# Kernel optimization log

Hardware: AMD Instinct MI355X
Metric: run time of the kernel (lower is better)

## Reference

```python
import jax, jax.numpy as jnp
import numpy as np

N_NODES = 50000
N_EDGES = 800000
HIDDEN = 128
BN_EPS = 1e-5


def setup_inputs() -> dict:
    key = jax.random.key(0)
    k_h, k_e, k_wl, k_wr = jax.random.split(key, 4)
    h = jax.random.normal(k_h, (N_NODES, HIDDEN), dtype=jnp.float32)
    edge_index = jax.random.randint(k_e, (2, N_EDGES), 0, N_NODES, dtype=jnp.int32)
    W_l = jax.random.normal(k_wl, (HIDDEN, HIDDEN), dtype=jnp.float32) / np.sqrt(HIDDEN)
    b_l = jnp.zeros((HIDDEN,), dtype=jnp.float32)
    W_r = jax.random.normal(k_wr, (HIDDEN, HIDDEN), dtype=jnp.float32) / np.sqrt(HIDDEN)
    gamma = jnp.ones((HIDDEN,), dtype=jnp.float32)
    beta = jnp.zeros((HIDDEN,), dtype=jnp.float32)
    return {"h": h, "edge_index": edge_index, "W_l": W_l, "b_l": b_l,
            "W_r": W_r, "gamma": gamma, "beta": beta}


def reference(h, edge_index, W_l, b_l, W_r, gamma, beta):
    # SAGEConv(aggr='mean'): out_i = W_l @ mean_{j->i} h_j + b_l + W_r @ h_i
    src = edge_index[0]  # message sources
    dst = edge_index[1]  # message targets
    n = h.shape[0]
    msg_sum = jax.ops.segment_sum(h[src], dst, num_segments=n)          # [N, D]
    deg = jax.ops.segment_sum(jnp.ones_like(dst, dtype=h.dtype), dst, num_segments=n)
    agg = msg_sum / jnp.maximum(deg, 1.0)[:, None]                      # mean aggregation
    out = agg @ W_l.T + b_l + h @ W_r.T                                 # [N, D]
    # BatchNorm1d (training mode: batch statistics, biased variance)
    mean = jnp.mean(out, axis=0)
    var = jnp.var(out, axis=0)
    out = gamma * (out - mean) * jax.lax.rsqrt(var + BN_EPS) + beta
    out = jax.nn.relu(out)
    # dropout p=0.0 -> identity; residual add
    return out + h
```

## Files before the change

kernel.cpp:

```cpp
#include <hip/hip_runtime.h>

#define N_NODES 50000
#define N_EDGES 800000
#define HIDDEN  128
#define BN_EPS  1e-5f
#define SLOT    64

__global__ __launch_bounds__(256) void bin_kernel(
    const int* __restrict__ edge_index,
    int* __restrict__ cnt,
    int* __restrict__ slots,
    float* __restrict__ bn_acc)
{
    if (blockIdx.x == 0) bn_acc[threadIdx.x] = 0.0f;

    const int* src = edge_index;
    const int* dst = edge_index + N_EDGES;
    const int e = blockIdx.x * blockDim.x + threadIdx.x;
    if (e < N_EDGES) {
        const int d = dst[e];
        const int s = src[e];
        const int pos = atomicAdd(&cnt[d], 1);
        if (pos < SLOT) slots[(size_t)d * SLOT + pos] = s;
    }
}

__global__ __launch_bounds__(256) void gather_kernel(
    const float* __restrict__ h,
    const int* __restrict__ cnt,
    const int* __restrict__ slots,
    float* __restrict__ agg)
{
    const int lane = threadIdx.x & 63;
    const int wave = (blockIdx.x * blockDim.x + threadIdx.x) >> 6;
    if (wave >= N_NODES) return;
    const int n = wave;

    int c = cnt[n];
    c = (c > SLOT) ? SLOT : c;
    const int* sl = slots + (size_t)n * SLOT;
    const int fo = lane * 2;

    float2 acc = make_float2(0.0f, 0.0f);
    int j = 0;
    for (; j + 8 <= c; j += 8) {
        int s0 = sl[j], s1 = sl[j+1], s2 = sl[j+2], s3 = sl[j+3];
        int s4 = sl[j+4], s5 = sl[j+5], s6 = sl[j+6], s7 = sl[j+7];
        float2 v0 = *reinterpret_cast<const float2*>(h + (size_t)s0 * HIDDEN + fo);
        float2 v1 = *reinterpret_cast<const float2*>(h + (size_t)s1 * HIDDEN + fo);
        float2 v2 = *reinterpret_cast<const float2*>(h + (size_t)s2 * HIDDEN + fo);
        float2 v3 = *reinterpret_cast<const float2*>(h + (size_t)s3 * HIDDEN + fo);
        float2 v4 = *reinterpret_cast<const float2*>(h + (size_t)s4 * HIDDEN + fo);
        float2 v5 = *reinterpret_cast<const float2*>(h + (size_t)s5 * HIDDEN + fo);
        float2 v6 = *reinterpret_cast<const float2*>(h + (size_t)s6 * HIDDEN + fo);
        float2 v7 = *reinterpret_cast<const float2*>(h + (size_t)s7 * HIDDEN + fo);
        acc.x += (v0.x + v1.x) + (v2.x + v3.x) + ((v4.x + v5.x) + (v6.x + v7.x));
        acc.y += (v0.y + v1.y) + (v2.y + v3.y) + ((v4.y + v5.y) + (v6.y + v7.y));
    }
    for (; j < c; j++) {
        const int s0 = sl[j];
        const float2 v0 = *reinterpret_cast<const float2*>(h + (size_t)s0 * HIDDEN + fo);
        acc.x += v0.x;
        acc.y += v0.y;
    }
    const float inv = 1.0f / (float)((c > 0) ? c : 1);
    acc.x *= inv;
    acc.y *= inv;
    *reinterpret_cast<float2*>(agg + (size_t)n * HIDDEN + fo) = acc;
}

#define BR 64
#define BC 128
#define KC 16

__global__ __launch_bounds__(256) void gemm_kernel(
    const float* __restrict__ agg,
    const float* __restrict__ h,
    const float* __restrict__ W_l,
    const float* __restrict__ b_l,
    const float* __restrict__ W_r,
    float* __restrict__ out,
    float* __restrict__ bn_acc)
{
    __shared__ float Xs[KC][BR];
    __shared__ float Ws[KC][BC];
    __shared__ float red[16][BC];

    const int tid  = threadIdx.x;
    const int row0 = blockIdx.x * BR;
    const int ty = tid >> 4;
    const int tx = tid & 15;

    float acc[4][8];
#pragma unroll
    for (int i = 0; i < 4; i++)
#pragma unroll
        for (int j = 0; j < 8; j++) acc[i][j] = 0.0f;

    const int srow = tid >> 2;
    const int sq   = (tid & 3) * 4;
    const int wcol = tid >> 1;
    const int wq   = (tid & 1) * 8;

    for (int kc = 0; kc < 2 * HIDDEN; kc += KC) {
        const float* X = (kc < HIDDEN) ? agg : h;
        const float* W = (kc < HIDDEN) ? W_l : W_r;
        const int kb = (kc & (HIDDEN - 1));

        {
            const int r = row0 + srow;
            float4 v = make_float4(0.f, 0.f, 0.f, 0.f);
            if (r < N_NODES)
                v = *reinterpret_cast<const float4*>(X + (size_t)r * HIDDEN + kb + sq);
            Xs[sq + 0][srow] = v.x; Xs[sq + 1][srow] = v.y;
            Xs[sq + 2][srow] = v.z; Xs[sq + 3][srow] = v.w;
        }
        {
            const float4* p = reinterpret_cast<const float4*>(W + (size_t)wcol * HIDDEN + kb + wq);
            float4 a = p[0], b = p[1];
            Ws[wq + 0][wcol] = a.x; Ws[wq + 1][wcol] = a.y;
            Ws[wq + 2][wcol] = a.z; Ws[wq + 3][wcol] = a.w;
            Ws[wq + 4][wcol] = b.x; Ws[wq + 5][wcol] = b.y;
            Ws[wq + 6][wcol] = b.z; Ws[wq + 7][wcol] = b.w;
        }
        __syncthreads();

#pragma unroll
        for (int kk = 0; kk < KC; kk++) {
            float4 av = *reinterpret_cast<const float4*>(&Xs[kk][ty * 4]);
            float4 b0 = *reinterpret_cast<const float4*>(&Ws[kk][tx * 4]);
            float4 b1 = *reinterpret_cast<const float4*>(&Ws[kk][64 + tx * 4]);
            float a[4] = {av.x, av.y, av.z, av.w};
            float b[8] = {b0.x, b0.y, b0.z, b0.w, b1.x, b1.y, b1.z, b1.w};
#pragma unroll
            for (int i = 0; i < 4; i++)
#pragma unroll
                for (int j = 0; j < 8; j++)
                    acc[i][j] += a[i] * b[j];
        }
        __syncthreads();
    }

    float4 bb0 = *reinterpret_cast<const float4*>(&b_l[tx * 4]);
    float4 bb1 = *reinterpret_cast<const float4*>(&b_l[64 + tx * 4]);
    float s[8], s2[8];
#pragma unroll
    for (int j = 0; j < 8; j++) { s[j] = 0.0f; s2[j] = 0.0f; }

#pragma unroll
    for (int i = 0; i < 4; i++) {
        const int r = row0 + ty * 4 + i;
        if (r < N_NODES) {
            float o[8];
            o[0] = acc[i][0] + bb0.x; o[1] = acc[i][1] + bb0.y;
            o[2] = acc[i][2] + bb0.z; o[3] = acc[i][3] + bb0.w;
            o[4] = acc[i][4] + bb1.x; o[5] = acc[i][5] + bb1.y;
            o[6] = acc[i][6] + bb1.z; o[7] = acc[i][7] + bb1.w;
            float* op = out + (size_t)r * HIDDEN;
            *reinterpret_cast<float4*>(op + tx * 4)      = make_float4(o[0], o[1], o[2], o[3]);
            *reinterpret_cast<float4*>(op + 64 + tx * 4) = make_float4(o[4], o[5], o[6], o[7]);
#pragma unroll
            for (int j = 0; j < 8; j++) { s[j] += o[j]; s2[j] += o[j] * o[j]; }
        }
    }

#pragma unroll
    for (int j = 0; j < 4; j++) {
        red[ty][tx * 4 + j]      = s[j];
        red[ty][64 + tx * 4 + j] = s[4 + j];
    }
    __syncthreads();
    if (tid < BC) {
        float t = 0.0f;
#pragma unroll
        for (int y = 0; y < 16; y++) t += red[y][tid];
        atomicAdd(&bn_acc[tid], t);
    }
    __syncthreads();
#pragma unroll
    for (int j = 0; j < 4; j++) {
        red[ty][tx * 4 + j]      = s2[j];
        red[ty][64 + tx * 4 + j] = s2[4 + j];
    }
    __syncthreads();
    if (tid < BC) {
        float t = 0.0f;
#pragma unroll
        for (int y = 0; y < 16; y++) t += red[y][tid];
        atomicAdd(&bn_acc[BC + tid], t);
    }
}

__global__ __launch_bounds__(256) void bn_apply_kernel(
    const float* __restrict__ h,
    const float* __restrict__ gamma,
    const float* __restrict__ beta,
    const float* __restrict__ bn_acc,
    float* __restrict__ out)
{
    const float inv_n = 1.0f / (float)N_NODES;
    const size_t total = (size_t)N_NODES * HIDDEN;
    size_t idx = ((size_t)blockIdx.x * blockDim.x + threadIdx.x) * 4;
    const size_t stride = (size_t)gridDim.x * blockDim.x * 4;

    for (; idx < total; idx += stride) {
        const int col = (int)(idx & (HIDDEN - 1));
        float4 x  = *reinterpret_cast<float4*>(out + idx);
        float4 sm = *reinterpret_cast<const float4*>(bn_acc + col);
        float4 sq = *reinterpret_cast<const float4*>(bn_acc + HIDDEN + col);
        float4 g  = *reinterpret_cast<const float4*>(gamma + col);
        float4 bt = *reinterpret_cast<const float4*>(beta + col);
        float4 hr = *reinterpret_cast<const float4*>(h + idx);

        float4 res;
        {
            float m = sm.x * inv_n; float var = sq.x * inv_n - m * m;
            float rs = rsqrtf(var + BN_EPS);
            float v = g.x * (x.x - m) * rs + bt.x;
            res.x = fmaxf(v, 0.0f) + hr.x;
        }
        {
            float m = sm.y * inv_n; float var = sq.y * inv_n - m * m;
            float rs = rsqrtf(var + BN_EPS);
            float v = g.y * (x.y - m) * rs + bt.y;
            res.y = fmaxf(v, 0.0f) + hr.y;
        }
        {
            float m = sm.z * inv_n; float var = sq.z * inv_n - m * m;
            float rs = rsqrtf(var + BN_EPS);
            float v = g.z * (x.z - m) * rs + bt.z;
            res.z = fmaxf(v, 0.0f) + hr.z;
        }
        {
            float m = sm.w * inv_n; float var = sq.w * inv_n - m * m;
            float rs = rsqrtf(var + BN_EPS);
            float v = g.w * (x.w - m) * rs + bt.w;
            res.w = fmaxf(v, 0.0f) + hr.w;
        }
        *reinterpret_cast<float4*>(out + idx) = res;
    }
}

extern "C" void kernel_launch(void* const* d_in, const int* in_sizes, int n_in,
                              void* d_out, int out_size, void* d_ws, size_t ws_size,
                              hipStream_t stream)
{
    const float* h          = (const float*)d_in[0];
    const int*   edge_index = (const int*)d_in[1];
    const float* W_l        = (const float*)d_in[2];
    const float* b_l        = (const float*)d_in[3];
    const float* W_r        = (const float*)d_in[4];
    const float* gamma      = (const float*)d_in[5];
    const float* beta       = (const float*)d_in[6];
    float* out = (float*)d_out;

    char* ws = (char*)d_ws;
    int*   cnt    = (int*)ws;
    int*   slots  = cnt + N_NODES;
    float* agg    = (float*)(slots + (size_t)N_NODES * SLOT);
    float* bn_acc = agg + (size_t)N_NODES * HIDDEN;

    hipMemsetAsync(cnt, 0, (size_t)N_NODES * sizeof(int), stream);

    bin_kernel<<<(N_EDGES + 255) / 256, 256, 0, stream>>>(edge_index, cnt, slots, bn_acc);

    gather_kernel<<<(N_NODES + 3) / 4, 256, 0, stream>>>(h, cnt, slots, agg);

    const int gemm_blocks = (N_NODES + BR - 1) / BR;
    gemm_kernel<<<gemm_blocks, 256, 0, stream>>>(agg, h, W_l, b_l, W_r, out, bn_acc);

    bn_apply_kernel<<<2048, 256, 0, stream>>>(h, gamma, beta, bn_acc, out);
}
```

Baseline: 258.5 us.

## Use split-bf16 MFMA GEMM with pre-split weights and half-wave gather

Replaces the FP32 SIMT GEMM with bf16 MFMA 16x16x32 instructions, using a hi/lo split (three MFMAs per tile) to keep near-FP32 accuracy. The weights are pre-split into bf16 hi/lo arrays inside the binning kernel and staged in XOR-swizzled shared memory. Activations are converted to hi/lo on the fly. The gather kernel now assigns one node per half-wave with float4 loads, and BN partial sums go through shared-memory atomics. The tradeoff is three times as many matrix ops plus conversion work and non-coalesced scalar output stores, in exchange for matrix-core throughput.

```diff
diff --git a/kernel.cpp b/kernel.cpp
--- a/kernel.cpp
+++ b/kernel.cpp
@@ -6,20 +6,49 @@
 #define BN_EPS  1e-5f
 #define SLOT    64
 
+typedef __attribute__((ext_vector_type(8))) short short8;
+typedef __attribute__((ext_vector_type(4))) float f32x4;
+
+__device__ inline unsigned short f2bf(float x) {
+    unsigned u = __float_as_uint(x);
+    return (unsigned short)((u + 0x7FFFu + ((u >> 16) & 1u)) >> 16);
+}
+__device__ inline void cvt8(const float* x, short8& hi, short8& lo) {
+#pragma unroll
+    for (int i = 0; i < 8; i++) {
+        unsigned u = __float_as_uint(x[i]);
+        unsigned r = (u + 0x7FFFu + ((u >> 16) & 1u)) & 0xFFFF0000u;
+        hi[i] = (short)(r >> 16);
+        float res = x[i] - __uint_as_float(r);
+        lo[i] = (short)f2bf(res);
+    }
+}
+
 __global__ __launch_bounds__(256) void bin_kernel(
     const int* __restrict__ edge_index,
+    const float* __restrict__ W_l,
+    const float* __restrict__ W_r,
     int* __restrict__ cnt,
     int* __restrict__ slots,
+    unsigned short* __restrict__ WhiG,
+    unsigned short* __restrict__ WloG,
     float* __restrict__ bn_acc)
 {
-    if (blockIdx.x == 0) bn_acc[threadIdx.x] = 0.0f;
-
-    const int* src = edge_index;
-    const int* dst = edge_index + N_EDGES;
-    const int e = blockIdx.x * blockDim.x + threadIdx.x;
-    if (e < N_EDGES) {
-        const int d = dst[e];
-        const int s = src[e];
+    const int gid = blockIdx.x * 256 + threadIdx.x;
+    if (blockIdx.x < 128) {
+        const int n = gid >> 8;
+        const int k = gid & 255;
+        const float w = (k < 128) ? W_l[n * 128 + k] : W_r[n * 128 + (k - 128)];
+        unsigned u = __float_as_uint(w);
+        unsigned r = (u + 0x7FFFu + ((u >> 16) & 1u)) & 0xFFFF0000u;
+        WhiG[gid] = (unsigned short)(r >> 16);
+        WloG[gid] = f2bf(w - __uint_as_float(r));
+    }
+    if (blockIdx.x == 128) bn_acc[threadIdx.x] = 0.0f;
+
+    if (gid < N_EDGES) {
+        const int d = edge_index[N_EDGES + gid];
+        const int s = edge_index[gid];
         const int pos = atomicAdd(&cnt[d], 1);
         if (pos < SLOT) slots[(size_t)d * SLOT + pos] = s;
     }
@@ -31,163 +60,144 @@
     const int* __restrict__ slots,
     float* __restrict__ agg)
 {
-    const int lane = threadIdx.x & 63;
+    const int half = (threadIdx.x >> 5) & 1;
+    const int sub  = threadIdx.x & 31;
     const int wave = (blockIdx.x * blockDim.x + threadIdx.x) >> 6;
-    if (wave >= N_NODES) return;
-    const int n = wave;
+    const int n = wave * 2 + half;
+    if (n >= N_NODES) return;
 
     int c = cnt[n];
     c = (c > SLOT) ? SLOT : c;
     const int* sl = slots + (size_t)n * SLOT;
-    const int fo = lane * 2;
-
-    float2 acc = make_float2(0.0f, 0.0f);
+    const int fo = sub * 4;
+
+    float4 acc = make_float4(0.0f, 0.0f, 0.0f, 0.0f);
     int j = 0;
-    for (; j + 8 <= c; j += 8) {
-        int s0 = sl[j], s1 = sl[j+1], s2 = sl[j+2], s3 = sl[j+3];
-        int s4 = sl[j+4], s5 = sl[j+5], s6 = sl[j+6], s7 = sl[j+7];
-        float2 v0 = *reinterpret_cast<const float2*>(h + (size_t)s0 * HIDDEN + fo);
-        float2 v1 = *reinterpret_cast<const float2*>(h + (size_t)s1 * HIDDEN + fo);
-        float2 v2 = *reinterpret_cast<const float2*>(h + (size_t)s2 * HIDDEN + fo);
-        float2 v3 = *reinterpret_cast<const float2*>(h + (size_t)s3 * HIDDEN + fo);
-        float2 v4 = *reinterpret_cast<const float2*>(h + (size_t)s4 * HIDDEN + fo);
-        float2 v5 = *reinterpret_cast<const float2*>(h + (size_t)s5 * HIDDEN + fo);
-        float2 v6 = *reinterpret_cast<const float2*>(h + (size_t)s6 * HIDDEN + fo);
-        float2 v7 = *reinterpret_cast<const float2*>(h + (size_t)s7 * HIDDEN + fo);
-        acc.x += (v0.x + v1.x) + (v2.x + v3.x) + ((v4.x + v5.x) + (v6.x + v7.x));
-        acc.y += (v0.y + v1.y) + (v2.y + v3.y) + ((v4.y + v5.y) + (v6.y + v7.y));
+    for (; j + 4 <= c; j += 4) {
+        const int s0 = sl[j], s1 = sl[j + 1], s2 = sl[j + 2], s3 = sl[j + 3];
+        const float4 v0 = *reinterpret_cast<const float4*>(h + (size_t)s0 * HIDDEN + fo);
+        const float4 v1 = *reinterpret_cast<const float4*>(h + (size_t)s1 * HIDDEN + fo);
+        const float4 v2 = *reinterpret_cast<const float4*>(h + (size_t)s2 * HIDDEN + fo);
+        const float4 v3 = *reinterpret_cast<const float4*>(h + (size_t)s3 * HIDDEN + fo);
+        acc.x += (v0.x + v1.x) + (v2.x + v3.x);
+        acc.y += (v0.y + v1.y) + (v2.y + v3.y);
+        acc.z += (v0.z + v1.z) + (v2.z + v3.z);
+        acc.w += (v0.w + v1.w) + (v2.w + v3.w);
     }
     for (; j < c; j++) {
-        const int s0 = sl[j];
-        const float2 v0 = *reinterpret_cast<const float2*>(h + (size_t)s0 * HIDDEN + fo);
-        acc.x += v0.x;
-        acc.y += v0.y;
+        const float4 v0 = *reinterpret_cast<const float4*>(h + (size_t)sl[j] * HIDDEN + fo);
+        acc.x += v0.x; acc.y += v0.y; acc.z += v0.z; acc.w += v0.w;
     }
     const float inv = 1.0f / (float)((c > 0) ? c : 1);
-    acc.x *= inv;
-    acc.y *= inv;
-    *reinterpret_cast<float2*>(agg + (size_t)n * HIDDEN + fo) = acc;
-}
-
-#define BR 64
-#define BC 128
-#define KC 16
+    acc.x *= inv; acc.y *= inv; acc.z *= inv; acc.w *= inv;
+    *reinterpret_cast<float4*>(agg + (size_t)n * HIDDEN + fo) = acc;
+}
 
 __global__ __launch_bounds__(256) void gemm_kernel(
     const float* __restrict__ agg,
     const float* __restrict__ h,
-    const float* __restrict__ W_l,
+    const unsigned short* __restrict__ WhiG,
+    const unsigned short* __restrict__ WloG,
     const float* __restrict__ b_l,
-    const float* __restrict__ W_r,
     float* __restrict__ out,
     float* __restrict__ bn_acc)
 {
-    __shared__ float Xs[KC][BR];
-    __shared__ float Ws[KC][BC];
-    __shared__ float red[16][BC];
+    __shared__ short WsH[128][64];
+    __shared__ short WsL[128][64];
+    __shared__ float bnS[128];
+    __shared__ float bnS2[128];
 
     const int tid  = threadIdx.x;
-    const int row0 = blockIdx.x * BR;
-    const int ty = tid >> 4;
-    const int tx = tid & 15;
-
-    float acc[4][8];
-#pragma unroll
-    for (int i = 0; i < 4; i++)
-#pragma unroll
-        for (int j = 0; j < 8; j++) acc[i][j] = 0.0f;
-
-    const int srow = tid >> 2;
-    const int sq   = (tid & 3) * 4;
-    const int wcol = tid >> 1;
-    const int wq   = (tid & 1) * 8;
-
-    for (int kc = 0; kc < 2 * HIDDEN; kc += KC) {
-        const float* X = (kc < HIDDEN) ? agg : h;
-        const float* W = (kc < HIDDEN) ? W_l : W_r;
-        const int kb = (kc & (HIDDEN - 1));
-
-        {
-            const int r = row0 + srow;
-            float4 v = make_float4(0.f, 0.f, 0.f, 0.f);
-            if (r < N_NODES)
-                v = *reinterpret_cast<const float4*>(X + (size_t)r * HIDDEN + kb + sq);
-            Xs[sq + 0][srow] = v.x; Xs[sq + 1][srow] = v.y;
-            Xs[sq + 2][srow] = v.z; Xs[sq + 3][srow] = v.w;
-        }
-        {
-            const float4* p = reinterpret_cast<const float4*>(W + (size_t)wcol * HIDDEN + kb + wq);
-            float4 a = p[0], b = p[1];
-            Ws[wq + 0][wcol] = a.x; Ws[wq + 1][wcol] = a.y;
-            Ws[wq + 2][wcol] = a.z; Ws[wq + 3][wcol] = a.w;
-            Ws[wq + 4][wcol] = b.x; Ws[wq + 5][wcol] = b.y;
-            Ws[wq + 6][wcol] = b.z; Ws[wq + 7][wcol] = b.w;
-        }
+    const int lane = tid & 63;
+    const int wv   = tid >> 6;
+    const int row0 = blockIdx.x * 128;
+    const int colb = lane & 15;
+    const int quad = lane >> 4;
+
+    if (tid < 128) { bnS[tid] = 0.0f; bnS2[tid] = 0.0f; }
+
+    f32x4 acc[2][8];
+#pragma unroll
+    for (int s = 0; s < 2; s++)
+#pragma unroll
+        for (int c = 0; c < 8; c++) acc[s][c] = (f32x4)(0.0f);
+
+    const int wcol  = tid >> 1;
+    const int sbase = (tid & 1) * 4;
+
+    for (int kc = 0; kc < 4; kc++) {
+        const float* X = (kc < 2) ? agg : h;
+        const int kb = (kc & 1) * 64;
+        const int kw = kc * 64;
+
         __syncthreads();
-
-#pragma unroll
-        for (int kk = 0; kk < KC; kk++) {
-            float4 av = *reinterpret_cast<const float4*>(&Xs[kk][ty * 4]);
-            float4 b0 = *reinterpret_cast<const float4*>(&Ws[kk][tx * 4]);
-            float4 b1 = *reinterpret_cast<const float4*>(&Ws[kk][64 + tx * 4]);
-            float a[4] = {av.x, av.y, av.z, av.w};
-            float b[8] = {b0.x, b0.y, b0.z, b0.w, b1.x, b1.y, b1.z, b1.w};
-#pragma unroll
-            for (int i = 0; i < 4; i++)
-#pragma unroll
-                for (int j = 0; j < 8; j++)
-                    acc[i][j] += a[i] * b[j];
+#pragma unroll
+        for (int j = 0; j < 4; j++) {
+            const int slot = sbase + j;
+            short8 vh = *reinterpret_cast<const short8*>(WhiG + (size_t)wcol * 256 + kw + slot * 8);
+            short8 vl = *reinterpret_cast<const short8*>(WloG + (size_t)wcol * 256 + kw + slot * 8);
+            const int sp = slot ^ (wcol & 7);
+            *reinterpret_cast<short8*>(&WsH[wcol][sp * 8]) = vh;
+            *reinterpret_cast<short8*>(&WsL[wcol][sp * 8]) = vl;
         }
         __syncthreads();
-    }
-
-    float4 bb0 = *reinterpret_cast<const float4*>(&b_l[tx * 4]);
-    float4 bb1 = *reinterpret_cast<const float4*>(&b_l[64 + tx * 4]);
-    float s[8], s2[8];
-#pragma unroll
-    for (int j = 0; j < 8; j++) { s[j] = 0.0f; s2[j] = 0.0f; }
-
-#pragma unroll
-    for (int i = 0; i < 4; i++) {
-        const int r = row0 + ty * 4 + i;
-        if (r < N_NODES) {
-            float o[8];
-            o[0] = acc[i][0] + bb0.x; o[1] = acc[i][1] + bb0.y;
-            o[2] = acc[i][2] + bb0.z; o[3] = acc[i][3] + bb0.w;
-            o[4] = acc[i][4] + bb1.x; o[5] = acc[i][5] + bb1.y;
-            o[6] = acc[i][6] + bb1.z; o[7] = acc[i][7] + bb1.w;
-            float* op = out + (size_t)r * HIDDEN;
-            *reinterpret_cast<float4*>(op + tx * 4)      = make_float4(o[0], o[1], o[2], o[3]);
-            *reinterpret_cast<float4*>(op + 64 + tx * 4) = make_float4(o[4], o[5], o[6], o[7]);
-#pragma unroll
-            for (int j = 0; j < 8; j++) { s[j] += o[j]; s2[j] += o[j] * o[j]; }
-        }
-    }
-
-#pragma unroll
-    for (int j = 0; j < 4; j++) {
-        red[ty][tx * 4 + j]      = s[j];
-        red[ty][64 + tx * 4 + j] = s[4 + j];
+
+#pragma unroll
+        for (int ks = 0; ks < 2; ks++) {
+            short8 ahi[2], alo[2];
+#pragma unroll
+            for (int sub = 0; sub < 2; sub++) {
+                int row = row0 + wv * 32 + sub * 16 + colb;
+                row = (row < N_NODES) ? row : (N_NODES - 1);
+                const float* xp = X + (size_t)row * HIDDEN + kb + ks * 32 + quad * 8;
+                float xr[8];
+                const float4 p0 = *reinterpret_cast<const float4*>(xp);
+                const float4 p1 = *reinterpret_cast<const float4*>(xp + 4);
+                xr[0] = p0.x; xr[1] = p0.y; xr[2] = p0.z; xr[3] = p0.w;
+                xr[4] = p1.x; xr[5] = p1.y; xr[6] = p1.z; xr[7] = p1.w;
+                cvt8(xr, ahi[sub], alo[sub]);
+            }
+#pragma unroll
+            for (int c = 0; c < 8; c++) {
+                const int bc = c * 16 + colb;
+                const int sp = (ks * 4 + quad) ^ (bc & 7);
+                short8 bhi = *reinterpret_cast<const short8*>(&WsH[bc][sp * 8]);
+                short8 blo = *reinterpret_cast<const short8*>(&WsL[bc][sp * 8]);
+#pragma unroll
+                for (int sub = 0; sub < 2; sub++) {
+                    acc[sub][c] = __builtin_amdgcn_mfma_f32_16x16x32_bf16(ahi[sub], bhi, acc[sub][c], 0, 0, 0);
+                    acc[sub][c] = __builtin_amdgcn_mfma_f32_16x16x32_bf16(ahi[sub], blo, acc[sub][c], 0, 0, 0);
+                    acc[sub][c] = __builtin_amdgcn_mfma_f32_16x16x32_bf16(alo[sub], bhi, acc[sub][c], 0, 0, 0);
+                }
+            }
+        }
+    }
+
+#pragma unroll
+    for (int c = 0; c < 8; c++) {
+        const int col = c * 16 + colb;
+        const float bias = b_l[col];
+        float s = 0.0f, s2 = 0.0f;
+#pragma unroll
+        for (int sub = 0; sub < 2; sub++) {
+            const int rbase = row0 + wv * 32 + sub * 16 + quad * 4;
+#pragma unroll
+            for (int reg = 0; reg < 4; reg++) {
+                const int r = rbase + reg;
+                if (r < N_NODES) {
+                    const float o = acc[sub][c][reg] + bias;
+                    out[(size_t)r * HIDDEN + col] = o;
+                    s += o; s2 += o * o;
+                }
+            }
+        }
+        atomicAdd(&bnS[col], s);
+        atomicAdd(&bnS2[col], s2);
     }
     __syncthreads();
-    if (tid < BC) {
-        float t = 0.0f;
-#pragma unroll
-        for (int y = 0; y < 16; y++) t += red[y][tid];
-        atomicAdd(&bn_acc[tid], t);
-    }
-    __syncthreads();
-#pragma unroll
-    for (int j = 0; j < 4; j++) {
-        red[ty][tx * 4 + j]      = s2[j];
-        red[ty][64 + tx * 4 + j] = s2[4 + j];
-    }
-    __syncthreads();
-    if (tid < BC) {
-        float t = 0.0f;
-#pragma unroll
-        for (int y = 0; y < 16; y++) t += red[y][tid];
-        atomicAdd(&bn_acc[BC + tid], t);
+    if (tid < 128) {
+        atomicAdd(&bn_acc[tid], bnS[tid]);
+        atomicAdd(&bn_acc[128 + tid], bnS2[tid]);
     }
 }
 
@@ -215,26 +225,22 @@
         float4 res;
         {
             float m = sm.x * inv_n; float var = sq.x * inv_n - m * m;
-            float rs = rsqrtf(var + BN_EPS);
-            float v = g.x * (x.x - m) * rs + bt.x;
+            float v = g.x * (x.x - m) * rsqrtf(var + BN_EPS) + bt.x;
             res.x = fmaxf(v, 0.0f) + hr.x;
         }
         {
             float m = sm.y * inv_n; float var = sq.y * inv_n - m * m;
-            float rs = rsqrtf(var + BN_EPS);
-            float v = g.y * (x.y - m) * rs + bt.y;
+            float v = g.y * (x.y - m) * rsqrtf(var + BN_EPS) + bt.y;
             res.y = fmaxf(v, 0.0f) + hr.y;
         }
         {
             float m = sm.z * inv_n; float var = sq.z * inv_n - m * m;
-            float rs = rsqrtf(var + BN_EPS);
-            float v = g.z * (x.z - m) * rs + bt.z;
+            float v = g.z * (x.z - m) * rsqrtf(var + BN_EPS) + bt.z;
             res.z = fmaxf(v, 0.0f) + hr.z;
         }
         {
             float m = sm.w * inv_n; float var = sq.w * inv_n - m * m;
-            float rs = rsqrtf(var + BN_EPS);
-            float v = g.w * (x.w - m) * rs + bt.w;
+            float v = g.w * (x.w - m) * rsqrtf(var + BN_EPS) + bt.w;
             res.w = fmaxf(v, 0.0f) + hr.w;
         }
         *reinterpret_cast<float4*>(out + idx) = res;
@@ -255,19 +261,22 @@
     float* out = (float*)d_out;
 
     char* ws = (char*)d_ws;
-    int*   cnt    = (int*)ws;
-    int*   slots  = cnt + N_NODES;
-    float* agg    = (float*)(slots + (size_t)N_NODES * SLOT);
-    float* bn_acc = agg + (size_t)N_NODES * HIDDEN;
+    int*   cnt   = (int*)ws;
+    int*   slots = cnt + N_NODES;
+    float* agg   = (float*)(slots + (size_t)N_NODES * SLOT);
+    unsigned short* WhiG = (unsigned short*)(agg + (size_t)N_NODES * HIDDEN);
+    unsigned short* WloG = WhiG + 128 * 256;
+    float* bn_acc = (float*)(WloG + 128 * 256);
 
     hipMemsetAsync(cnt, 0, (size_t)N_NODES * sizeof(int), stream);
 
-    bin_kernel<<<(N_EDGES + 255) / 256, 256, 0, stream>>>(edge_index, cnt, slots, bn_acc);
-
-    gather_kernel<<<(N_NODES + 3) / 4, 256, 0, stream>>>(h, cnt, slots, agg);
-
-    const int gemm_blocks = (N_NODES + BR - 1) / BR;
-    gemm_kernel<<<gemm_blocks, 256, 0, stream>>>(agg, h, W_l, b_l, W_r, out, bn_acc);
+    bin_kernel<<<(N_EDGES + 255) / 256, 256, 0, stream>>>(
+        edge_index, W_l, W_r, cnt, slots, WhiG, WloG, bn_acc);
+
+    gather_kernel<<<(N_NODES / 2 + 3) / 4, 256, 0, stream>>>(h, cnt, slots, agg);
+
+    gemm_kernel<<<(N_NODES + 127) / 128, 256, 0, stream>>>(
+        agg, h, WhiG, WloG, b_l, out, bn_acc);
 
     bn_apply_kernel<<<2048, 256, 0, stream>>>(h, gamma, beta, bn_acc, out);
 }
```

Result: faster. 237.9 us (-8.0%).
